# Kernel tuning notes

Hardware: AMD Instinct MI355X
Metric: run time of the kernel (lower is better)

Reference implementation:

```python
import jax, jax.numpy as jnp
import numpy as np

N_NODES = 50000
D_IN = 128
D_OUT = 128
N_EDGES = 800000


def setup_inputs() -> dict:
    key = jax.random.key(0)
    k1, k2, k3, k4 = jax.random.split(key, 4)
    x = jax.random.normal(k1, (N_NODES, D_IN), dtype=jnp.float32)
    # nn.Linear(input_size, output_size, bias=False): weight is [out, in], y = x @ W.T.
    # We store W1 as [in, out] so y = x @ W1 (same math, transposed storage).
    W1 = jax.random.normal(k2, (D_IN, D_OUT), dtype=jnp.float32) * (1.0 / np.sqrt(D_IN))
    row = jax.random.randint(k3, (N_EDGES,), 0, N_NODES, dtype=jnp.int64)
    col = jax.random.randint(k4, (N_EDGES,), 0, N_NODES, dtype=jnp.int64)
    edge_index = jnp.stack([row, col], axis=0)  # [2, E]
    return {"x": x, "W1": W1, "edge_index": edge_index}


def reference(x, W1, edge_index):
    # Linear transform: [N, D_in] @ [D_in, D_out] -> [N, D_out]
    norm_m = x @ W1
    adj_row = edge_index[0]  # source nodes (gather)
    adj_col = edge_index[1]  # destination nodes (scatter)
    gathered = norm_m[adj_row]  # [E, D_out]
    pooled = jax.ops.segment_max(gathered, adj_col, num_segments=x.shape[0])
    # torch_scatter fills segments with no incoming edges with 0 (not -inf)
    deg = jax.ops.segment_sum(jnp.ones_like(adj_col, dtype=jnp.int32), adj_col,
                              num_segments=x.shape[0])
    pooled = jnp.where((deg > 0)[:, None], pooled, jnp.zeros_like(pooled))
    return jnp.concatenate((x, pooled), axis=1)  # [N, D_in + D_out]
```

## Files before the change

### kernel.cpp

```cpp
#include <hip/hip_runtime.h>


#define N_DIN 128
#define CAP 64

typedef __attribute__((ext_vector_type(8))) short bf16x8;
typedef __attribute__((ext_vector_type(4))) float f32x4;

__device__ __forceinline__ short f32_bf16(float f) {
    unsigned u = __float_as_uint(f);
    return (short)((u + 0x7fffu + ((u >> 16) & 1u)) >> 16);
}

__device__ __forceinline__ unsigned ctr_val(unsigned raw) {
    unsigned a = raw - 0xAAAAAAAAu;
    return a < raw ? a : raw;
}

__global__ __launch_bounds__(256) void fused_k(const float* __restrict__ X,
                                               const float* __restrict__ W,
                                               short* __restrict__ Yb,
                                               float* __restrict__ out, int N, int gblocks,
                                               const int* __restrict__ row,
                                               const int* __restrict__ col,
                                               unsigned* __restrict__ cur,
                                               unsigned short* __restrict__ csrc, int E) {
    __shared__ short lds[128 * 128];
    if ((int)blockIdx.x >= gblocks) {
        int e = ((int)blockIdx.x - gblocks) * 256 + (int)threadIdx.x;
        if (e < E) {
            int dst = col[e];
            unsigned pos = ctr_val(atomicAdd(&cur[dst], 1u));
            if (pos < CAP)
                csrc[dst * CAP + pos] = (unsigned short)row[e];
        }
        return;
    }
    const int tid = threadIdx.x;
    {
        int n = tid >> 1;
        int kh = (tid & 1) * 64;
#pragma unroll
        for (int c = 0; c < 8; ++c) {
            int k0 = kh + c * 8;
            short tmp[8];
#pragma unroll
            for (int j = 0; j < 8; ++j)
                tmp[j] = f32_bf16(W[(k0 + j) * 128 + n]);
            *(bf16x8*)(&lds[n * 128 + k0]) = *(const bf16x8*)tmp;
        }
    }
    const int w = tid >> 6, l = tid & 63;
    const int lr = l & 15, lg = l >> 4;
    const int R0 = (int)blockIdx.x * 128 + w * 32;

    bf16x8 af[2][4];
#pragma unroll
    for (int rt = 0; rt < 2; ++rt) {
        int gr = R0 + rt * 16 + lr;
        int grc = gr < N ? gr : N - 1;
#pragma unroll
        for (int t = 0; t < 4; ++t) {
            int kc = t * 32 + lg * 8;
            float4 v0 = *(const float4*)(X + (size_t)grc * 128 + kc);
            float4 v1 = *(const float4*)(X + (size_t)grc * 128 + kc + 4);
            if (gr < N) {
                *(float4*)(out + (size_t)gr * 256 + kc)     = v0;
                *(float4*)(out + (size_t)gr * 256 + kc + 4) = v1;
            }
            bf16x8 a;
            a[0] = f32_bf16(v0.x); a[1] = f32_bf16(v0.y);
            a[2] = f32_bf16(v0.z); a[3] = f32_bf16(v0.w);
            a[4] = f32_bf16(v1.x); a[5] = f32_bf16(v1.y);
            a[6] = f32_bf16(v1.z); a[7] = f32_bf16(v1.w);
            af[rt][t] = a;
        }
    }
    __syncthreads();

    f32x4 acc0[8], acc1[8];
#pragma unroll
    for (int ct = 0; ct < 8; ++ct) { acc0[ct] = (f32x4){0,0,0,0}; acc1[ct] = (f32x4){0,0,0,0}; }
#pragma unroll
    for (int ct = 0; ct < 8; ++ct) {
        const short* bp = &lds[(ct * 16 + lr) * 128];
#pragma unroll
        for (int t = 0; t < 4; ++t) {
            bf16x8 b = *(const bf16x8*)(bp + t * 32 + lg * 8);
            acc0[ct] = __builtin_amdgcn_mfma_f32_16x16x32_bf16(af[0][t], b, acc0[ct], 0, 0, 0);
            acc1[ct] = __builtin_amdgcn_mfma_f32_16x16x32_bf16(af[1][t], b, acc1[ct], 0, 0, 0);
        }
    }
    __syncthreads();
    short (*cl)[128] = (short(*)[128])(lds + w * 32 * 128);
#pragma unroll
    for (int ct = 0; ct < 8; ++ct)
#pragma unroll
        for (int i = 0; i < 4; ++i) {
            cl[lg * 4 + i][ct * 16 + lr]      = f32_bf16(acc0[ct][i]);
            cl[16 + lg * 4 + i][ct * 16 + lr] = f32_bf16(acc1[ct][i]);
        }
#pragma unroll
    for (int it = 0; it < 8; ++it) {
        int cid = it * 64 + l;
        int r2 = cid >> 4, c2 = cid & 15;
        int gr = R0 + r2;
        if (gr < N) {
            bf16x8 vv = *(const bf16x8*)(&cl[r2][c2 * 8]);
            *(bf16x8*)(Yb + (size_t)gr * 128 + c2 * 8) = vv;
        }
    }
}

__global__ __launch_bounds__(256) void pool_k(const unsigned* __restrict__ nmb,
                                              const unsigned* __restrict__ cur,
                                              const unsigned short* __restrict__ csrc,
                                              float* __restrict__ out, int N) {
    int node = blockIdx.x * 4 + (threadIdx.x >> 6);
    if (node >= N) return;
    int lane = threadIdx.x & 63;
    int half = lane >> 5, sl = lane & 31;
    unsigned deg = ctr_val(cur[node]);
    if (deg > CAP) deg = CAP;
    int mysrc = csrc[node * CAP + lane];
    float4 acc = make_float4(-INFINITY, -INFINITY, -INFINITY, -INFINITY);
    unsigned j = 0;
    for (; j + 8 <= deg; j += 8) {
        uint2 v[4];
#pragma unroll
        for (int i = 0; i < 4; ++i) {
            int s = __shfl(mysrc, (int)(j + 2 * i + half), 64);
            v[i] = *(const uint2*)(nmb + (size_t)s * 64 + sl * 2);
        }
#pragma unroll
        for (int i = 0; i < 4; ++i) {
            acc.x = fmaxf(acc.x, __uint_as_float(v[i].x << 16));
            acc.y = fmaxf(acc.y, __uint_as_float(v[i].x & 0xffff0000u));
            acc.z = fmaxf(acc.z, __uint_as_float(v[i].y << 16));
            acc.w = fmaxf(acc.w, __uint_as_float(v[i].y & 0xffff0000u));
        }
    }
    for (; j + 2 <= deg; j += 2) {
        int s = __shfl(mysrc, (int)(j + half), 64);
        uint2 v = *(const uint2*)(nmb + (size_t)s * 64 + sl * 2);
        acc.x = fmaxf(acc.x, __uint_as_float(v.x << 16));
        acc.y = fmaxf(acc.y, __uint_as_float(v.x & 0xffff0000u));
        acc.z = fmaxf(acc.z, __uint_as_float(v.y << 16));
        acc.w = fmaxf(acc.w, __uint_as_float(v.y & 0xffff0000u));
    }
    if (j < deg) {
        int s = __shfl(mysrc, (int)j, 64);
        uint2 v = *(const uint2*)(nmb + (size_t)s * 64 + sl * 2);
        acc.x = fmaxf(acc.x, __uint_as_float(v.x << 16));
        acc.y = fmaxf(acc.y, __uint_as_float(v.x & 0xffff0000u));
        acc.z = fmaxf(acc.z, __uint_as_float(v.y << 16));
        acc.w = fmaxf(acc.w, __uint_as_float(v.y & 0xffff0000u));
    }
    acc.x = fmaxf(acc.x, __shfl_xor(acc.x, 32, 64));
    acc.y = fmaxf(acc.y, __shfl_xor(acc.y, 32, 64));
    acc.z = fmaxf(acc.z, __shfl_xor(acc.z, 32, 64));
    acc.w = fmaxf(acc.w, __shfl_xor(acc.w, 32, 64));
    if (deg == 0) acc = make_float4(0.f, 0.f, 0.f, 0.f);
    if (half == 0)
        *(float4*)(out + (size_t)node * 256 + N_DIN + sl * 4) = acc;
}

extern "C" void kernel_launch(void* const* d_in, const int* in_sizes, int n_in,
                              void* d_out, int out_size, void* d_ws, size_t ws_size,
                              hipStream_t stream) {
    const float* x  = (const float*)d_in[0];
    const float* W1 = (const float*)d_in[1];
    const int* ei   = (const int*)d_in[2];
    const int N = in_sizes[0] / N_DIN;
    const int E = in_sizes[2] / 2;
    const int* row = ei;
    const int* col = ei + E;
    float* out = (float*)d_out;

    short* norm_mb = (short*)d_ws;
    unsigned* cur = (unsigned*)(norm_mb + (size_t)N * N_DIN);
    unsigned short* csrc = (unsigned short*)(cur + N);

    const int gblocks = (N + 127) / 128;
    const int sblocks = (E + 255) / 256;

    fused_k<<<gblocks + sblocks, 256, 0, stream>>>(x, W1, norm_mb, out, N, gblocks,
                                                   row, col, cur, csrc, E);
    pool_k<<<(N + 3) / 4, 256, 0, stream>>>((const unsigned*)norm_mb, cur, csrc, out, N);
}
```

Baseline: 157.3 us.

## Drop LDS staging in GEMM; read W directly and store results per lane

Removes the 32KB shared-memory buffer used to stage bf16 W and to transpose outputs. Each lane now loads W from global memory, converts it to bf16 for every MFMA tile, and writes 2-byte results straight to global memory. The aim is higher occupancy (launch bounds of 8 blocks per CU), fewer barriers and fewer live accumulator registers. In exchange, W is loaded and converted redundantly by every wave, and output stores become scattered 16-bit writes instead of 128-bit coalesced rows.

Result: slower. 231.9 us (+47.4%).

```diff
diff --git a/kernel.cpp b/kernel.cpp
--- a/kernel.cpp
+++ b/kernel.cpp
@@ -17,15 +17,14 @@
     return a < raw ? a : raw;
 }
 
-__global__ __launch_bounds__(256) void fused_k(const float* __restrict__ X,
-                                               const float* __restrict__ W,
-                                               short* __restrict__ Yb,
-                                               float* __restrict__ out, int N, int gblocks,
-                                               const int* __restrict__ row,
-                                               const int* __restrict__ col,
-                                               unsigned* __restrict__ cur,
-                                               unsigned short* __restrict__ csrc, int E) {
-    __shared__ short lds[128 * 128];
+__global__ __launch_bounds__(256, 8) void fused_k(const float* __restrict__ X,
+                                                  const float* __restrict__ W,
+                                                  short* __restrict__ Yb,
+                                                  float* __restrict__ out, int N, int gblocks,
+                                                  const int* __restrict__ row,
+                                                  const int* __restrict__ col,
+                                                  unsigned* __restrict__ cur,
+                                                  unsigned short* __restrict__ csrc, int E) {
     if ((int)blockIdx.x >= gblocks) {
         int e = ((int)blockIdx.x - gblocks) * 256 + (int)threadIdx.x;
         if (e < E) {
@@ -37,19 +36,6 @@
         return;
     }
     const int tid = threadIdx.x;
-    {
-        int n = tid >> 1;
-        int kh = (tid & 1) * 64;
-#pragma unroll
-        for (int c = 0; c < 8; ++c) {
-            int k0 = kh + c * 8;
-            short tmp[8];
-#pragma unroll
-            for (int j = 0; j < 8; ++j)
-                tmp[j] = f32_bf16(W[(k0 + j) * 128 + n]);
-            *(bf16x8*)(&lds[n * 128 + k0]) = *(const bf16x8*)tmp;
-        }
-    }
     const int w = tid >> 6, l = tid & 63;
     const int lr = l & 15, lg = l >> 4;
     const int R0 = (int)blockIdx.x * 128 + w * 32;
@@ -76,38 +62,27 @@
             af[rt][t] = a;
         }
     }
-    __syncthreads();
 
-    f32x4 acc0[8], acc1[8];
-#pragma unroll
-    for (int ct = 0; ct < 8; ++ct) { acc0[ct] = (f32x4){0,0,0,0}; acc1[ct] = (f32x4){0,0,0,0}; }
 #pragma unroll
     for (int ct = 0; ct < 8; ++ct) {
-        const short* bp = &lds[(ct * 16 + lr) * 128];
+        f32x4 c0 = {0.f, 0.f, 0.f, 0.f}, c1 = {0.f, 0.f, 0.f, 0.f};
+        const float* wp = W + ct * 16 + lr;
 #pragma unroll
         for (int t = 0; t < 4; ++t) {
-            bf16x8 b = *(const bf16x8*)(bp + t * 32 + lg * 8);
-            acc0[ct] = __builtin_amdgcn_mfma_f32_16x16x32_bf16(af[0][t], b, acc0[ct], 0, 0, 0);
-            acc1[ct] = __builtin_amdgcn_mfma_f32_16x16x32_bf16(af[1][t], b, acc1[ct], 0, 0, 0);
+            int k0 = t * 32 + lg * 8;
+            bf16x8 b;
+#pragma unroll
+            for (int j = 0; j < 8; ++j)
+                b[j] = f32_bf16(wp[(size_t)(k0 + j) * 128]);
+            c0 = __builtin_amdgcn_mfma_f32_16x16x32_bf16(af[0][t], b, c0, 0, 0, 0);
+            c1 = __builtin_amdgcn_mfma_f32_16x16x32_bf16(af[1][t], b, c1, 0, 0, 0);
         }
-    }
-    __syncthreads();
-    short (*cl)[128] = (short(*)[128])(lds + w * 32 * 128);
-#pragma unroll
-    for (int ct = 0; ct < 8; ++ct)
 #pragma unroll
         for (int i = 0; i < 4; ++i) {
-            cl[lg * 4 + i][ct * 16 + lr]      = f32_bf16(acc0[ct][i]);
-            cl[16 + lg * 4 + i][ct * 16 + lr] = f32_bf16(acc1[ct][i]);
-        }
-#pragma unroll
-    for (int it = 0; it < 8; ++it) {
-        int cid = it * 64 + l;
-        int r2 = cid >> 4, c2 = cid & 15;
-        int gr = R0 + r2;
-        if (gr < N) {
-            bf16x8 vv = *(const bf16x8*)(&cl[r2][c2 * 8]);
-            *(bf16x8*)(Yb + (size_t)gr * 128 + c2 * 8) = vv;
+            int r0 = R0 + lg * 4 + i;
+            int r1 = r0 + 16;
+            if (r0 < N) Yb[(size_t)r0 * 128 + ct * 16 + lr] = f32_bf16(c0[i]);
+            if (r1 < N) Yb[(size_t)r1 * 128 + ct * 16 + lr] = f32_bf16(c1[i]);
         }
     }
 }
```
